# Kernel optimization log

Measured on AMD Instinct MI355X. Metric: run time of the kernel, lower is better.

Reference implementation:

```python
import jax, jax.numpy as jnp
import numpy as np
import math

B, D, N, H, NHEADS, NCLS = 4096, 256, 256, 1, 4, 10


def conv(x, w, b, stride, pad):
    y = jax.lax.conv_general_dilated(x, w, (stride, stride), [(pad, pad), (pad, pad)],
                                     dimension_numbers=('NCHW', 'OIHW', 'NCHW'))
    return y + b[None, :, None, None]


def cdist(z, c):
    # z: [B, D], c: [N, D] -> Euclidean distance [B, N]
    d2 = jnp.sum(z * z, -1)[:, None] + jnp.sum(c * c, -1)[None, :] - 2.0 * (z @ c.T)
    return jnp.sqrt(jnp.maximum(d2, 0.0))


def setup_inputs() -> dict:
    key = jax.random.key(0)
    ks = jax.random.split(key, 32)
    s = 0.02
    inp = {
        'x': jax.random.normal(ks[0], (B, 3, 32, 32), jnp.float32),
        'y': jax.random.randint(ks[1], (B,), 0, NCLS),
        'conv1_w': jax.random.normal(ks[2], (32, 3, 5, 5), jnp.float32) * s,
        'conv1_b': jnp.zeros((32,), jnp.float32),
        'conv2_w': jax.random.normal(ks[3], (64, 32, 3, 3), jnp.float32) * s,
        'conv2_b': jnp.zeros((64,), jnp.float32),
        'conv3_w': jax.random.normal(ks[4], (128, 64, 3, 3), jnp.float32) * s,
        'conv3_b': jnp.zeros((128,), jnp.float32),
        'conv4_w': jax.random.normal(ks[5], (256, 128, 3, 3), jnp.float32) * s,
        'conv4_b': jnp.zeros((256,), jnp.float32),
        'enc_w': jax.random.normal(ks[6], (256 * 8 * 8, D), jnp.float32) * s,
        'enc_b': jnp.zeros((D,), jnp.float32),
        'class_emb': jax.random.normal(ks[7], (NCLS, D), jnp.float32),
        'node_emb': jax.random.normal(ks[8], (N_NODES := 1, D), jnp.float32),
        'query_w': jax.random.normal(ks[9], (D, D), jnp.float32) * s,
        'query_b': jnp.zeros((D,), jnp.float32),
        'attn_w': jax.random.normal(ks[10], (D, D * NHEADS), jnp.float32) * s,
        'attn_b': jnp.zeros((D * NHEADS,), jnp.float32),
        'clf_w': jax.random.normal(ks[11], (D * NHEADS, NCLS), jnp.float32) * s,
        'clf_b': jnp.zeros((NCLS,), jnp.float32),
        'node_fc_w': jax.random.normal(ks[12], (D, D), jnp.float32) * s,
        'node_fc_b': jnp.zeros((D,), jnp.float32),
        'protos': jax.random.normal(ks[13], (N, D), jnp.float32),
        'grid_pos': jax.random.normal(ks[14], (N, D), jnp.float32),
        'temp_raw': jnp.array([math.log(0.95 / 0.05)], jnp.float32),
        'gate_logits': jnp.zeros((N,), jnp.float32),
    }
    return inp


def reference(x, y, conv1_w, conv1_b, conv2_w, conv2_b, conv3_w, conv3_b,
              conv4_w, conv4_b, enc_w, enc_b, class_emb, node_emb,
              query_w, query_b, attn_w, attn_b, clf_w, clf_b,
              node_fc_w, node_fc_b, protos, grid_pos, temp_raw, gate_logits):
    # shared encoder: conv stack -> flatten -> linear, 32x32 -> 8x8
    h1 = jax.nn.relu(conv(x, conv1_w, conv1_b, 2, 1))    # [B,32,15,15]
    h2 = jax.nn.relu(conv(h1, conv2_w, conv2_b, 2, 1))   # [B,64,8,8]
    h3 = jax.nn.relu(conv(h2, conv3_w, conv3_b, 1, 1))   # [B,128,8,8]
    h4 = jax.nn.relu(conv(h3, conv4_w, conv4_b, 1, 1))   # [B,256,8,8]
    z0 = h4.reshape(x.shape[0], -1) @ enc_w + enc_b      # [B,D]

    # Node: encoder_fc + SoftSOM (cdist + cdist -> softmax -> gate -> renorm -> blend)
    z = z0 @ node_fc_w + node_fc_b
    temp = jax.nn.sigmoid(temp_raw[0]) * (1.0 - 0.001) + 0.001
    d_total = cdist(z, protos) + cdist(z, grid_pos)      # [B,N]
    w = jax.nn.softmax(-d_total / temp, axis=-1) * jax.nn.sigmoid(gate_logits)[None, :]
    w = w / (w.sum(-1, keepdims=True) + 1e-8)
    blended = w @ protos                                 # [B,D]

    # node attention over n_nodes=1
    topo_stack = blended[:, None, :]                     # [B,1,D]
    query = class_emb[y] @ query_w + query_b             # [B,D]
    proj = (node_emb @ attn_w + attn_b).reshape(node_emb.shape[0], NHEADS, D)  # [n,h,D]
    attn_logits = jnp.einsum('bd,nhd->bhn', query, proj)
    attn_w_ = jax.nn.softmax(attn_logits, axis=-1)
    fused = jnp.einsum('bhn,bnd->bhd', attn_w_, topo_stack).reshape(x.shape[0], NHEADS * D)
    logits = fused @ clf_w + clf_b                       # [B,10]
    return logits
```

## Files before the change

kernel.cpp:

```cpp
#include <hip/hip_runtime.h>
#include <math.h>

#define TPB 256

typedef __attribute__((ext_vector_type(8))) short bf16x8;
typedef __attribute__((ext_vector_type(4))) float f32x4;
typedef __attribute__((ext_vector_type(2))) float f32x2;

#define OFF_PN2   0
#define OFF_GN2   256
#define OFF_GATE  512
#define OFF_TEMP  768
#define OFF_WEFF  1024
#define OFF_W1T   3584
#define OFF_W2T_BYTES 737280ul
#define OFF_W3T_BYTES 786432ul
#define OFF_W4T_BYTES 983040ul
#define OFF_EWT_BYTES 2097152ul
#define OFF_NFWT_BYTES 10485760ul
#define OFF_PJD_BYTES  10616832ul
#define OFF_GJD_BYTES  10747904ul
#define OFF_PTB_BYTES  10878976ul
#define OFF_A_BYTES   12582912ul
#define OFF_B_BYTES   (OFF_A_BYTES + 67108864ul)
#define OFF_Z0_BYTES  (OFF_B_BYTES + 33554432ul)

__device__ __forceinline__ float bf2f(ushort u) {
  return __uint_as_float(((unsigned)u) << 16);
}
__device__ __forceinline__ ushort f2bf(float f) {
  unsigned x = __float_as_uint(f);
  return (ushort)((x + 0x7fffu + ((x >> 16) & 1u)) >> 16);
}
__device__ __forceinline__ unsigned pack2(float a, float b) {
  return (unsigned)f2bf(a) | ((unsigned)f2bf(b) << 16);
}

__device__ __forceinline__ void gload_lds16(const ushort* g, ushort* l) {
  __builtin_amdgcn_global_load_lds(
      (const __attribute__((address_space(1))) unsigned int*)g,
      (__attribute__((address_space(3))) unsigned int*)l, 16, 0, 0);
}

__device__ __forceinline__ float block_sum(float v, float* red) {
  #pragma unroll
  for (int off = 32; off > 0; off >>= 1) v += __shfl_down(v, off, 64);
  int wid = threadIdx.x >> 6;
  __syncthreads();
  if ((threadIdx.x & 63) == 0) red[wid] = v;
  __syncthreads();
  return red[0] + red[1] + red[2] + red[3];
}

__global__ void __launch_bounds__(256) k_init(
    const float* __restrict__ ew,    ushort* __restrict__ ewt,
    const float* __restrict__ w1,    const float* __restrict__ w2,
    const float* __restrict__ w3,    const float* __restrict__ w4,
    float* __restrict__ w1t, ushort* __restrict__ w2t,
    ushort* __restrict__ w3t, ushort* __restrict__ w4t,
    const float* __restrict__ protos, const float* __restrict__ gridp,
    const float* __restrict__ gate_logits, const float* __restrict__ temp_raw,
    const float* __restrict__ clf_w, float* __restrict__ ws,
    float* __restrict__ z0,
    const float* __restrict__ nfw, ushort* __restrict__ nfwt,
    ushort* __restrict__ pjd, ushort* __restrict__ gjd,
    ushort* __restrict__ ptb) {
  __shared__ float tile[64][65];
  __shared__ float red[4];
  const int bx = blockIdx.x, t = threadIdx.x;

  if (bx < 1024) {
    int kb = bx & 255, nb = bx >> 8;
    #pragma unroll
    for (int i = 0; i < 16; ++i) {
      int idx = t + i*256, k = idx >> 6, n = idx & 63;
      tile[k][n] = ew[(size_t)(kb*64 + k)*256 + nb*64 + n];
    }
    __syncthreads();
    #pragma unroll
    for (int i = 0; i < 16; ++i) {
      int idx = t + i*256, n = idx >> 6, k = idx & 63;
      ewt[(size_t)(nb*64 + n)*16384 + kb*64 + k] = f2bf(tile[k][n]);
    }
    return;
  }
  if (bx < 2176) {
    int idx = (bx - 1024)*256 + t;
    if (idx < 2400) {
      int tap = idx >> 5, oc = idx & 31;
      w1t[idx] = w1[oc*75 + tap];
    }
    if (idx < 18432) {
      int tap = idx >> 11, r = idx & 2047, oc = r >> 5, ic = r & 31;
      w2t[idx] = f2bf(w2[oc*288 + ic*9 + tap]);
    }
    if (idx < 73728) {
      int tap = idx >> 13, r = idx & 8191, oc = r >> 6, ic = r & 63;
      w3t[idx] = f2bf(w3[oc*576 + ic*9 + tap]);
    }
    if (idx < 294912) {
      int tap = idx >> 15, r = idx & 32767, oc = r >> 7, ic = r & 127;
      w4t[idx] = f2bf(w4[oc*1152 + ic*9 + tap]);
    }
    return;
  }
  if (bx < 2432) {
    int b = bx - 2176;
    #pragma unroll
    for (int u = 0; u < 16; ++u) z0[(size_t)u*65536 + b*256 + t] = 0.f;
    float pv = protos[b*256 + t];
    float gv = gridp [b*256 + t];
    float sp = block_sum(pv*pv, red);
    float sg = block_sum(gv*gv, red);
    if (t == 0) {
      ws[OFF_PN2 + b] = sp;
      ws[OFF_GN2 + b] = sg;
      ws[OFF_GATE + b] = 1.f/(1.f + expf(-gate_logits[b]));
    }
    if (b == 0) {
      for (int i = t; i < 2560; i += TPB) {
        int d = i/10, c = i%10;
        ws[OFF_WEFF + i] = clf_w[d*10+c] + clf_w[(256+d)*10+c]
                         + clf_w[(512+d)*10+c] + clf_w[(768+d)*10+c];
      }
      if (t == 0) {
        float s = 1.f/(1.f + expf(-temp_raw[0]));
        ws[OFF_TEMP] = s*(1.f - 0.001f) + 0.001f;
      }
    }
    return;
  }
  {
    int idx = (bx - 2432)*256 + t;
    int a = idx >> 8, b = idx & 255;
    nfwt[idx] = f2bf(nfw[b*256 + a]);
    pjd [idx] = f2bf(protos[idx]);
    gjd [idx] = f2bf(gridp[idx]);
    ptb [idx] = f2bf(protos[b*256 + a]);
  }
}

__global__ void __launch_bounds__(256) k_conv12(const float* __restrict__ x,
    const float* __restrict__ w1t, const float* __restrict__ b1,
    const ushort* __restrict__ w2t, const float* __restrict__ b2,
    ushort* __restrict__ h2c) {
  __shared__ ushort xs[17*17*40];
  __shared__ float  xf[3*32*33];
  int b = blockIdx.x, t = threadIdx.x;
  for (int i = t; i < 5780; i += TPB) ((unsigned*)xs)[i] = 0u;
  const float* xb = x + (size_t)b*3072;
  #pragma unroll
  for (int i = 0; i < 3; ++i) {
    int idx = (t + i*256)*4;
    float4 v = *(const float4*)&xb[idx];
    int ic = idx >> 10, rem = idx & 1023, iy = rem >> 5, ix = rem & 31;
    float* dst = &xf[ic*1056 + iy*33 + ix];
    dst[0] = v.x; dst[1] = v.y; dst[2] = v.z; dst[3] = v.w;
  }
  __syncthreads();

  if (t < 225) {
    int oy = t/15, ox = t%15;
    f32x2 acc[16];
    #pragma unroll
    for (int o = 0; o < 16; ++o) acc[o] = *(const f32x2*)&b1[2*o];
    for (int ic = 0; ic < 3; ++ic) {
      const int icb = ic*1056;
      #pragma unroll
      for (int ky = 0; ky < 5; ++ky) {
        int iy = 2*oy - 1 + ky;
        bool rok = (unsigned)iy < 32u;
        int rbase = icb + (rok ? iy*33 : 0);
        #pragma unroll
        for (int kx = 0; kx < 5; ++kx) {
          int ix = 2*ox - 1 + kx;
          bool ok = rok && ((unsigned)ix < 32u);
          float xv = xf[rbase + (ok ? ix : 0)];
          xv = ok ? xv : 0.f;
          f32x2 xv2 = {xv, xv};
          const float* wrow = &w1t[(ic*25 + ky*5 + kx)*32];
          #pragma unroll
          for (int g = 0; g < 8; ++g) {
            f32x2 wlo = {wrow[4*g+0], wrow[4*g+1]};
            f32x2 whi = {wrow[4*g+2], wrow[4*g+3]};
            acc[2*g]   += xv2*wlo;
            acc[2*g+1] += xv2*whi;
          }
        }
      }
    }
    unsigned pk[16];
    #pragma unroll
    for (int g = 0; g < 16; ++g)
      pk[g] = pack2(fmaxf(acc[g].x, 0.f), fmaxf(acc[g].y, 0.f));
    ushort* cell = &xs[((oy+1)*17 + (ox+1))*40];
    #pragma unroll
    for (int q = 0; q < 4; ++q) *(uint4*)(cell + q*8) = ((uint4*)pk)[q];
  }
  __syncthreads();

  const int lane = t & 63, w = t >> 6;
  const int quad = lane >> 4, row16 = lane & 15;
  f32x4 acc2[4];
  #pragma unroll
  for (int mt = 0; mt < 4; ++mt) acc2[mt] = (f32x4)0.f;
  #pragma unroll
  for (int ky = 0; ky < 3; ++ky)
    #pragma unroll
    for (int kx = 0; kx < 3; ++kx) {
      int tap = ky*3 + kx;
      bf16x8 bf = *(const bf16x8*)&w2t[tap*2048 + (w*16 + row16)*32 + quad*8];
      #pragma unroll
      for (int mt = 0; mt < 4; ++mt) {
        int px = mt*16 + row16;
        int iy = 2*(px >> 3) + ky, ix = 2*(px & 7) + kx;
        bf16x8 af = *(const bf16x8*)&xs[(iy*17 + ix)*40 + quad*8];
        acc2[mt] = __builtin_amdgcn_mfma_f32_16x16x32_bf16(bf, af, acc2[mt], 0, 0, 0);
      }
    }
  float4 bb = *(const float4*)&b2[w*16 + quad*4];
  #pragma unroll
  for (int mt = 0; mt < 4; ++mt) {
    int px = mt*16 + row16;
    uint2 dd;
    dd.x = pack2(fmaxf(acc2[mt][0] + bb.x, 0.f), fmaxf(acc2[mt][1] + bb.y, 0.f));
    dd.y = pack2(fmaxf(acc2[mt][2] + bb.z, 0.f), fmaxf(acc2[mt][3] + bb.w, 0.f));
    *(uint2*)&h2c[(size_t)b*4096 + px*64 + w*16 + quad*4] = dd;
  }
}

__global__ void __launch_bounds__(256, 2) k_conv34(const ushort* __restrict__ h2c,
    const float* __restrict__ b3, const float* __restrict__ b4,
    const ushort* __restrict__ w3t, const ushort* __restrict__ w4t,
    ushort* __restrict__ h4c, int img_base) {
  __shared__ __attribute__((aligned(16))) ushort buf[27200];
  ushort* xp  = buf;
  ushort* h3p = buf;
  const int bl = blockIdx.x, t = threadIdx.x;

  for (int i = t; i < 648; i += 256) {
    int img = (i >= 324), r = i - img*324;
    int row = r/9, c = r - row*9;
    int rr = (row < 20) ? ((row < 10) ? row : row + 80)
                        : (((row-20) >> 1) + 1)*10 + ((row-20) & 1)*9;
    *(uint4*)&xp[img*7200 + rr*72 + c*8] = (uint4){0,0,0,0};
  }
  #pragma unroll
  for (int u = 0; u < 4; ++u) {
    int i = t + u*256;
    int img = i >> 9, px = (i >> 3) & 63, icg = i & 7;
    bf16x8 v = *(const bf16x8*)&h2c[(size_t)(img_base + bl*2 + img)*4096 + px*64 + icg*8];
    int row = ((px >> 3) + 1)*10 + (px & 7) + 1;
    *(bf16x8*)&xp[img*7200 + row*72 + icg*8] = v;
  }
  __syncthreads();

  const int lane = t & 63, w = t >> 6;
  const int quad = lane >> 4, row16 = lane & 15;

  int b3off[8], b4off[8], r11c[8];
  #pragma unroll
  for (int mt = 0; mt < 8; ++mt) {
    int px = (mt & 3)*16 + row16;
    int r00 = (px >> 3)*10 + (px & 7);
    int img = mt >> 2;
    b3off[mt] = img*7200  + r00*72  + quad*8;
    b4off[mt] = img*13600 + r00*136 + quad*8;
    r11c[mt]  = img*13600 + (r00 + 11)*136;
  }

  const int ocb3 = w*32;
  f32x4 c3[8][2];
  #pragma unroll
  for (int mt = 0; mt < 8; ++mt) { c3[mt][0] = (f32x4)0.f; c3[mt][1] = (f32x4)0.f; }
  const ushort* w3b = w3t + (ocb3 + row16)*64 + quad*8;
  bf16x8 wa0 = *(const bf16x8*)(w3b);
  bf16x8 wa1 = *(const bf16x8*)(w3b + 1024);
  #pragma unroll
  for (int tap = 0; tap < 9; ++tap) {
    const int t72 = ((tap/3)*10 + (tap%3))*72;
    #pragma unroll
    for (int ks = 0; ks < 2; ++ks) {
      const ushort* wn = w3b + ((ks == 0) ? (tap*8192 + 32) : ((tap+1)*8192));
      bf16x8 n0 = *(const bf16x8*)(wn);
      bf16x8 n1 = *(const bf16x8*)(wn + 1024);
      #pragma unroll
      for (int mt = 0; mt < 8; ++mt) {
        bf16x8 af = *(const bf16x8*)&xp[b3off[mt] + t72 + ks*32];
        c3[mt][0] = __builtin_amdgcn_mfma_f32_16x16x32_bf16(wa0, af, c3[mt][0], 0, 0, 0);
        c3[mt][1] = __builtin_amdgcn_mfma_f32_16x16x32_bf16(wa1, af, c3[mt][1], 0, 0, 0);
      }
      wa0 = n0; wa1 = n1;
    }
  }
  __syncthreads();

  for (int i = t; i < 1224; i += 256) {
    int img2 = (i >= 612), r = i - img2*612;
    int row = r/17, c = r - row*17;
    int rr = (row < 20) ? ((row < 10) ? row : row + 80)
                        : (((row-20) >> 1) + 1)*10 + ((row-20) & 1)*9;
    *(uint4*)&h3p[img2*13600 + rr*136 + c*8] = (uint4){0,0,0,0};
  }
  #pragma unroll
  for (int nt = 0; nt < 2; ++nt) {
    float4 bb = *(const float4*)&b3[ocb3 + nt*16 + quad*4];
    #pragma unroll
    for (int mt = 0; mt < 8; ++mt) {
      uint2 dd;
      dd.x = pack2(fmaxf(c3[mt][nt][0] + bb.x, 0.f), fmaxf(c3[mt][nt][1] + bb.y, 0.f));
      dd.y = pack2(fmaxf(c3[mt][nt][2] + bb.z, 0.f), fmaxf(c3[mt][nt][3] + bb.w, 0.f));
      *(uint2*)&h3p[r11c[mt] + ocb3 + nt*16 + quad*4] = dd;
    }
  }
  __syncthreads();

  const int ocb4 = w*64;
  f32x4 c4[8][4];
  #pragma unroll
  for (int mt = 0; mt < 8; ++mt)
    #pragma unroll
    for (int nt = 0; nt < 4; ++nt) c4[mt][nt] = (f32x4)0.f;
  const ushort* w4b = w4t + (ocb4 + row16)*128 + quad*8;
  bf16x8 r4[4];
  #pragma unroll
  for (int nt = 0; nt < 4; ++nt) r4[nt] = *(const bf16x8*)(w4b + nt*2048);
  #pragma unroll
  for (int tap = 0; tap < 9; ++tap) {
    const int t136 = ((tap/3)*10 + (tap%3))*136;
    #pragma unroll
    for (int ks = 0; ks < 4; ++ks) {
      const ushort* wn = w4b + ((ks < 3) ? (tap*32768 + (ks+1)*32) : ((tap+1)*32768));
      bf16x8 nx[4];
      #pragma unroll
      for (int nt = 0; nt < 4; ++nt) nx[nt] = *(const bf16x8*)(wn + nt*2048);
      #pragma unroll
      for (int mt = 0; mt < 8; ++mt) {
        bf16x8 ax = *(const bf16x8*)&h3p[b4off[mt] + t136 + ks*32];
        #pragma unroll
        for (int nt = 0; nt < 4; ++nt)
          c4[mt][nt] = __builtin_amdgcn_mfma_f32_16x16x32_bf16(ax, r4[nt], c4[mt][nt], 0, 0, 0);
      }
      #pragma unroll
      for (int nt = 0; nt < 4; ++nt) r4[nt] = nx[nt];
    }
  }
  #pragma unroll
  for (int nt = 0; nt < 4; ++nt) {
    int oc = ocb4 + nt*16 + row16;
    float bv = b4[oc];
    #pragma unroll
    for (int mt = 0; mt < 8; ++mt) {
      int ig = bl*2 + (mt >> 2);
      int px0 = (mt & 3)*16 + quad*4;
      uint2 dd;
      dd.x = pack2(fmaxf(c4[mt][nt][0] + bv, 0.f), fmaxf(c4[mt][nt][1] + bv, 0.f));
      dd.y = pack2(fmaxf(c4[mt][nt][2] + bv, 0.f), fmaxf(c4[mt][nt][3] + bv, 0.f));
      *(uint2*)&h4c[(size_t)ig*16384 + oc*64 + px0] = dd;
    }
  }
}

__global__ void __launch_bounds__(256) k_enc(const ushort* __restrict__ h4c,
    const ushort* __restrict__ ewt, float* __restrict__ z0, int img_base) {
  __shared__ ushort a_s[2][128*64];
  __shared__ ushort b_s[2][128*64];
  const int t = threadIdx.x, bid = blockIdx.x;
  const int grp = (bid & 7) + ((bid >> 7) << 3);
  const int slice = grp & 15;
  const int nb    = grp >> 4;
  const int mb    = (bid >> 3) & 15;
  const int M0 = mb*128, N0 = nb*128;
  const int kbase = slice*1024;
  const int lane = t & 63, wv = t >> 6;
  const int quad = lane >> 4, row16 = lane & 15;
  const int mrow0 = (wv & 1)*64, ncol0 = (wv >> 1)*64;
  const int sr = lane >> 3, sp = lane & 7;

  f32x4 acc[4][4];
  #pragma unroll
  for (int mt = 0; mt < 4; ++mt)
    #pragma unroll
    for (int nt = 0; nt < 4; ++nt) acc[mt][nt] = (f32x4)0.f;

  #pragma unroll
  for (int u = 0; u < 4; ++u) {
    int r = wv*32 + u*8 + sr;
    int c = sp ^ (r & 7);
    gload_lds16(&h4c[(size_t)(M0 + r)*16384 + kbase + c*8], &a_s[0][(wv*32 + u*8)*64]);
    gload_lds16(&ewt[(size_t)(N0 + r)*16384 + kbase + c*8], &b_s[0][(wv*32 + u*8)*64]);
  }
  __syncthreads();

  int cur = 0;
  for (int kt = 0; kt < 16; ++kt) {
    if (kt < 15) {
      const int k1 = kbase + (kt + 1)*64;
      #pragma unroll
      for (int u = 0; u < 4; ++u) {
        int r = wv*32 + u*8 + sr;
        int c = sp ^ (r & 7);
        gload_lds16(&h4c[(size_t)(M0 + r)*16384 + k1 + c*8], &a_s[cur^1][(wv*32 + u*8)*64]);
        gload_lds16(&ewt[(size_t)(N0 + r)*16384 + k1 + c*8], &b_s[cur^1][(wv*32 + u*8)*64]);
      }
    }
    #pragma unroll
    for (int ks = 0; ks < 2; ++ks) {
      bf16x8 af[4], bf[4];
      #pragma unroll
      for (int mt = 0; mt < 4; ++mt) {
        int r = mrow0 + mt*16 + row16;
        int p = (ks*4 + quad) ^ (r & 7);
        af[mt] = *(const bf16x8*)&a_s[cur][r*64 + p*8];
      }
      #pragma unroll
      for (int nt = 0; nt < 4; ++nt) {
        int r = ncol0 + nt*16 + row16;
        int p = (ks*4 + quad) ^ (r & 7);
        bf[nt] = *(const bf16x8*)&b_s[cur][r*64 + p*8];
      }
      #pragma unroll
      for (int mt = 0; mt < 4; ++mt)
        #pragma unroll
        for (int nt = 0; nt < 4; ++nt)
          acc[mt][nt] = __builtin_amdgcn_mfma_f32_16x16x32_bf16(af[mt], bf[nt], acc[mt][nt], 0, 0, 0);
    }
    __syncthreads();
    cur ^= 1;
  }
  #pragma unroll
  for (int mt = 0; mt < 4; ++mt) {
    int mrow = M0 + mrow0 + mt*16 + quad*4;
    #pragma unroll
    for (int nt = 0; nt < 4; ++nt) {
      int col = N0 + ncol0 + nt*16 + row16;
      #pragma unroll
      for (int r = 0; r < 4; ++r)
        atomicAdd(&z0[(size_t)(img_base + mrow + r)*256 + col], acc[mt][nt][r]);
    }
  }
}

__global__ void __launch_bounds__(256) k_post2(const float* __restrict__ z0,
    const float* __restrict__ enc_b, const float* __restrict__ nfb,
    const ushort* __restrict__ nfwt, const ushort* __restrict__ pjd,
    const ushort* __restrict__ gjd, const ushort* __restrict__ ptb,
    const float* __restrict__ ws, const float* __restrict__ clf_b,
    float* __restrict__ out) {
  __shared__ ushort zin[16*264];
  __shared__ ushort zS [16*264];
  __shared__ float  Df [16*264];
  __shared__ ushort wS [16*264];
  __shared__ float  weffS[2560];
  __shared__ float  gateS[256], pnS[256], gnS[256];
  __shared__ float  z2s[16];
  const int t = threadIdx.x, bx = blockIdx.x;
  const int img0 = bx*16;
  gateS[t] = ws[OFF_GATE + t];
  pnS[t]   = ws[OFF_PN2 + t];
  gnS[t]   = ws[OFF_GN2 + t];
  #pragma unroll
  for (int u = 0; u < 10; ++u)
    weffS[t + u*256] = ws[OFF_WEFF + t + u*256];
  #pragma unroll
  for (int u = 0; u < 16; ++u) {
    int i = t + u*256;
    int im = i >> 8, d = i & 255;
    zin[im*264 + d] = f2bf(z0[(size_t)(img0 + im)*256 + d] + enc_b[d]);
  }
  __syncthreads();

  const int lane = t & 63, w = t >> 6;
  const int quad = lane >> 4, row16 = lane & 15;
  const int n0 = w*64;

  f32x4 zC[4];
  #pragma unroll
  for (int nt = 0; nt < 4; ++nt) zC[nt] = (f32x4)0.f;
  #pragma unroll
  for (int ks = 0; ks < 8; ++ks) {
    bf16x8 az = *(const bf16x8*)&zin[row16*264 + ks*32 + quad*8];
    #pragma unroll
    for (int nt = 0; nt < 4; ++nt) {
      bf16x8 bw = *(const bf16x8*)&nfwt[(n0 + nt*16 + row16)*256 + ks*32 + quad*8];
      zC[nt] = __builtin_amdgcn_mfma_f32_16x16x32_bf16(az, bw, zC[nt], 0, 0, 0);
    }
  }
  #pragma unroll
  for (int nt = 0; nt < 4; ++nt) {
    int n = n0 + nt*16 + row16;
    float nb = nfb[n];
    #pragma unroll
    for (int r = 0; r < 4; ++r)
      zS[(quad*4 + r)*264 + n] = f2bf(zC[nt][r] + nb);
  }
  __syncthreads();

  {
    int im = t >> 4, jg = t & 15;
    float s = 0.f;
    #pragma unroll
    for (int q = 0; q < 16; ++q) {
      float v = bf2f(zS[im*264 + jg + 16*q]);
      s += v*v;
    }
    #pragma unroll
    for (int off = 8; off; off >>= 1) s += __shfl_xor(s, off, 16);
    if (jg == 0) z2s[im] = s;
  }
  __syncthreads();

  f32x4 dpC[4], dgC[4];
  #pragma unroll
  for (int nt = 0; nt < 4; ++nt) { dpC[nt] = (f32x4)0.f; dgC[nt] = (f32x4)0.f; }
  #pragma unroll
  for (int ks = 0; ks < 8; ++ks) {
    bf16x8 az = *(const bf16x8*)&zS[row16*264 + ks*32 + quad*8];
    #pragma unroll
    for (int nt = 0; nt < 4; ++nt) {
      int j = n0 + nt*16 + row16;
      bf16x8 bp = *(const bf16x8*)&pjd[j*256 + ks*32 + quad*8];
      bf16x8 bg = *(const bf16x8*)&gjd[j*256 + ks*32 + quad*8];
      dpC[nt] = __builtin_amdgcn_mfma_f32_16x16x32_bf16(az, bp, dpC[nt], 0, 0, 0);
      dgC[nt] = __builtin_amdgcn_mfma_f32_16x16x32_bf16(az, bg, dgC[nt], 0, 0, 0);
    }
  }
  {
    float temp = ws[OFF_TEMP];
    #pragma unroll
    for (int nt = 0; nt < 4; ++nt) {
      int j = n0 + nt*16 + row16;
      float pn = pnS[j], gn = gnS[j];
      #pragma unroll
      for (int r = 0; r < 4; ++r) {
        int im = quad*4 + r;
        float z2 = z2s[im];
        float d2p = z2 + pn - 2.f*dpC[nt][r];
        float d2g = z2 + gn - 2.f*dgC[nt][r];
        float l = -(sqrtf(fmaxf(d2p, 0.f)) + sqrtf(fmaxf(d2g, 0.f)))/temp;
        Df[im*264 + j] = l;
      }
    }
  }
  __syncthreads();

  {
    int im = t >> 4, jg = t & 15;
    float m = -1e30f;
    #pragma unroll
    for (int q = 0; q < 16; ++q) m = fmaxf(m, Df[im*264 + jg + 16*q]);
    #pragma unroll
    for (int off = 8; off; off >>= 1) m = fmaxf(m, __shfl_xor(m, off, 16));
    float E = 0.f, S = 0.f, ev[16], gv[16];
    #pragma unroll
    for (int q = 0; q < 16; ++q) {
      int j = jg + 16*q;
      float e = expf(Df[im*264 + j] - m);
      float g = gateS[j];
      ev[q] = e; gv[q] = g;
      E += e; S += e*g;
    }
    #pragma unroll
    for (int off = 8; off; off >>= 1) {
      E += __shfl_xor(E, off, 16);
      S += __shfl_xor(S, off, 16);
    }
    float inv = 1.f/(S + 1e-8f*E);
    #pragma unroll
    for (int q = 0; q < 16; ++q)
      wS[im*264 + jg + 16*q] = f2bf(ev[q]*gv[q]*inv);
  }
  __syncthreads();

  f32x4 blC[4];
  #pragma unroll
  for (int nt = 0; nt < 4; ++nt) blC[nt] = (f32x4)0.f;
  #pragma unroll
  for (int ks = 0; ks < 8; ++ks) {
    bf16x8 aw = *(const bf16x8*)&wS[row16*264 + ks*32 + quad*8];
    #pragma unroll
    for (int nt = 0; nt < 4; ++nt) {
      bf16x8 bp = *(const bf16x8*)&ptb[(n0 + nt*16 + row16)*256 + ks*32 + quad*8];
      blC[nt] = __builtin_amdgcn_mfma_f32_16x16x32_bf16(aw, bp, blC[nt], 0, 0, 0);
    }
  }
  #pragma unroll
  for (int nt = 0; nt < 4; ++nt) {
    int d = n0 + nt*16 + row16;
    #pragma unroll
    for (int r = 0; r < 4; ++r)
      Df[(quad*4 + r)*264 + d] = blC[nt][r];
  }
  __syncthreads();

  if (t < 160) {
    int im = t/10, c = t - im*10;
    float s = clf_b[c];
    for (int d = 0; d < 256; ++d)
      s += Df[im*264 + d]*weffS[d*10 + c];
    out[(size_t)(img0 + im)*10 + c] = s;
  }
}

extern "C" void kernel_launch(void* const* d_in, const int* in_sizes, int n_in,
                              void* d_out, int out_size, void* d_ws, size_t ws_size,
                              hipStream_t stream) {
  (void)in_sizes; (void)n_in; (void)out_size; (void)ws_size;
  const float* x      = (const float*)d_in[0];
  const float* c1w    = (const float*)d_in[2];
  const float* c1b    = (const float*)d_in[3];
  const float* c2w    = (const float*)d_in[4];
  const float* c2b    = (const float*)d_in[5];
  const float* c3w    = (const float*)d_in[6];
  const float* c3b    = (const float*)d_in[7];
  const float* c4w    = (const float*)d_in[8];
  const float* c4b    = (const float*)d_in[9];
  const float* encw   = (const float*)d_in[10];
  const float* encb   = (const float*)d_in[11];
  const float* clfw   = (const float*)d_in[18];
  const float* clfb   = (const float*)d_in[19];
  const float* nfw    = (const float*)d_in[20];
  const float* nfb    = (const float*)d_in[21];
  const float* protos = (const float*)d_in[22];
  const float* gridp  = (const float*)d_in[23];
  const float* traw   = (const float*)d_in[24];
  const float* gatel  = (const float*)d_in[25];

  float*  ws   = (float*)d_ws;
  float*  w1t  = ws + OFF_W1T;
  ushort* w2t  = (ushort*)((char*)d_ws + OFF_W2T_BYTES);
  ushort* w3t  = (ushort*)((char*)d_ws + OFF_W3T_BYTES);
  ushort* w4t  = (ushort*)((char*)d_ws + OFF_W4T_BYTES);
  ushort* ewt  = (ushort*)((char*)d_ws + OFF_EWT_BYTES);
  ushort* nfwt = (ushort*)((char*)d_ws + OFF_NFWT_BYTES);
  ushort* pjd  = (ushort*)((char*)d_ws + OFF_PJD_BYTES);
  ushort* gjd  = (ushort*)((char*)d_ws + OFF_GJD_BYTES);
  ushort* ptb  = (ushort*)((char*)d_ws + OFF_PTB_BYTES);
  ushort* h4c  = (ushort*)((char*)d_ws + OFF_A_BYTES);
  ushort* h2c  = (ushort*)((char*)d_ws + OFF_B_BYTES);
  float*  z0   = (float*) ((char*)d_ws + OFF_Z0_BYTES);
  float*  out  = (float*)d_out;

  hipLaunchKernelGGL(k_init, dim3(2688), dim3(TPB), 0, stream,
                     encw, ewt, c1w, c2w, c3w, c4w, w1t, w2t, w3t, w4t,
                     protos, gridp, gatel, traw, clfw, ws, z0,
                     nfw, nfwt, pjd, gjd, ptb);
  hipLaunchKernelGGL(k_conv12, dim3(4096), dim3(TPB), 0, stream, x, w1t, c1b, w2t, c2b, h2c);
  for (int c = 0; c < 2; ++c) {
    hipLaunchKernelGGL(k_conv34, dim3(1024), dim3(TPB), 0, stream,
                       h2c, c3b, c4b, w3t, w4t, h4c, c*2048);
    hipLaunchKernelGGL(k_enc, dim3(512), dim3(TPB), 0, stream, h4c, ewt, z0, c*2048);
  }
  hipLaunchKernelGGL(k_post2, dim3(256), dim3(TPB), 0, stream,
                     z0, encb, nfb, nfwt, pjd, gjd, ptb, ws, clfb, out);
}
```

Measured before the change: 518.9 us.

## Replace split-K atomic accumulation in encoder GEMM with partial buffers reduced in post

The encoder GEMM now uses 512-thread blocks, 8 K-slices of 2048 and 256 blocks per chunk. Each block writes its partial tile with plain stores into a per-slice buffer instead of doing fp32 atomicAdd into z0. k_post2 sums the 8 partials plus the bias when it loads z, so the z0 zero-init in k_init goes away. The aim is to remove atomic contention and the memset cost. In exchange, post-processing reads more memory, and the partial buffer reuses the already-consumed part of the h2c region.

```diff
diff --git a/kernel.cpp b/kernel.cpp
--- a/kernel.cpp
+++ b/kernel.cpp
@@ -61,7 +61,6 @@
     const float* __restrict__ protos, const float* __restrict__ gridp,
     const float* __restrict__ gate_logits, const float* __restrict__ temp_raw,
     const float* __restrict__ clf_w, float* __restrict__ ws,
-    float* __restrict__ z0,
     const float* __restrict__ nfw, ushort* __restrict__ nfwt,
     ushort* __restrict__ pjd, ushort* __restrict__ gjd,
     ushort* __restrict__ ptb) {
@@ -106,8 +105,6 @@
   }
   if (bx < 2432) {
     int b = bx - 2176;
-    #pragma unroll
-    for (int u = 0; u < 16; ++u) z0[(size_t)u*65536 + b*256 + t] = 0.f;
     float pv = protos[b*256 + t];
     float gv = gridp [b*256 + t];
     float sp = block_sum(pv*pv, red);
@@ -361,54 +358,53 @@
   }
 }
 
-__global__ void __launch_bounds__(256) k_enc(const ushort* __restrict__ h4c,
-    const ushort* __restrict__ ewt, float* __restrict__ z0, int img_base) {
+__global__ void __launch_bounds__(512) k_enc(const ushort* __restrict__ h4c,
+    const ushort* __restrict__ ewt, float* __restrict__ z0p) {
   __shared__ ushort a_s[2][128*64];
   __shared__ ushort b_s[2][128*64];
   const int t = threadIdx.x, bid = blockIdx.x;
-  const int grp = (bid & 7) + ((bid >> 7) << 3);
-  const int slice = grp & 15;
-  const int nb    = grp >> 4;
+  const int slice = bid & 7;
   const int mb    = (bid >> 3) & 15;
+  const int nb    = bid >> 7;
   const int M0 = mb*128, N0 = nb*128;
-  const int kbase = slice*1024;
+  const int kbase = slice*2048;
   const int lane = t & 63, wv = t >> 6;
   const int quad = lane >> 4, row16 = lane & 15;
-  const int mrow0 = (wv & 1)*64, ncol0 = (wv >> 1)*64;
+  const int mrow0 = (wv & 3)*32, ncol0 = (wv >> 2)*64;
   const int sr = lane >> 3, sp = lane & 7;
 
-  f32x4 acc[4][4];
-  #pragma unroll
-  for (int mt = 0; mt < 4; ++mt)
+  f32x4 acc[2][4];
+  #pragma unroll
+  for (int mt = 0; mt < 2; ++mt)
     #pragma unroll
     for (int nt = 0; nt < 4; ++nt) acc[mt][nt] = (f32x4)0.f;
 
   #pragma unroll
-  for (int u = 0; u < 4; ++u) {
-    int r = wv*32 + u*8 + sr;
+  for (int u = 0; u < 2; ++u) {
+    int r = wv*16 + u*8 + sr;
     int c = sp ^ (r & 7);
-    gload_lds16(&h4c[(size_t)(M0 + r)*16384 + kbase + c*8], &a_s[0][(wv*32 + u*8)*64]);
-    gload_lds16(&ewt[(size_t)(N0 + r)*16384 + kbase + c*8], &b_s[0][(wv*32 + u*8)*64]);
+    gload_lds16(&h4c[(size_t)(M0 + r)*16384 + kbase + c*8], &a_s[0][(wv*16 + u*8)*64]);
+    gload_lds16(&ewt[(size_t)(N0 + r)*16384 + kbase + c*8], &b_s[0][(wv*16 + u*8)*64]);
   }
   __syncthreads();
 
   int cur = 0;
-  for (int kt = 0; kt < 16; ++kt) {
-    if (kt < 15) {
+  for (int kt = 0; kt < 32; ++kt) {
+    if (kt < 31) {
       const int k1 = kbase + (kt + 1)*64;
       #pragma unroll
-      for (int u = 0; u < 4; ++u) {
-        int r = wv*32 + u*8 + sr;
+      for (int u = 0; u < 2; ++u) {
+        int r = wv*16 + u*8 + sr;
         int c = sp ^ (r & 7);
-        gload_lds16(&h4c[(size_t)(M0 + r)*16384 + k1 + c*8], &a_s[cur^1][(wv*32 + u*8)*64]);
-        gload_lds16(&ewt[(size_t)(N0 + r)*16384 + k1 + c*8], &b_s[cur^1][(wv*32 + u*8)*64]);
+        gload_lds16(&h4c[(size_t)(M0 + r)*16384 + k1 + c*8], &a_s[cur^1][(wv*16 + u*8)*64]);
+        gload_lds16(&ewt[(size_t)(N0 + r)*16384 + k1 + c*8], &b_s[cur^1][(wv*16 + u*8)*64]);
       }
     }
     #pragma unroll
     for (int ks = 0; ks < 2; ++ks) {
-      bf16x8 af[4], bf[4];
-      #pragma unroll
-      for (int mt = 0; mt < 4; ++mt) {
+      bf16x8 af[2], bf[4];
+      #pragma unroll
+      for (int mt = 0; mt < 2; ++mt) {
         int r = mrow0 + mt*16 + row16;
         int p = (ks*4 + quad) ^ (r & 7);
         af[mt] = *(const bf16x8*)&a_s[cur][r*64 + p*8];
@@ -420,7 +416,7 @@
         bf[nt] = *(const bf16x8*)&b_s[cur][r*64 + p*8];
       }
       #pragma unroll
-      for (int mt = 0; mt < 4; ++mt)
+      for (int mt = 0; mt < 2; ++mt)
         #pragma unroll
         for (int nt = 0; nt < 4; ++nt)
           acc[mt][nt] = __builtin_amdgcn_mfma_f32_16x16x32_bf16(af[mt], bf[nt], acc[mt][nt], 0, 0, 0);
@@ -429,19 +425,19 @@
     cur ^= 1;
   }
   #pragma unroll
-  for (int mt = 0; mt < 4; ++mt) {
-    int mrow = M0 + mrow0 + mt*16 + quad*4;
+  for (int mt = 0; mt < 2; ++mt) {
+    int il = M0 + mrow0 + mt*16 + quad*4;
     #pragma unroll
     for (int nt = 0; nt < 4; ++nt) {
       int col = N0 + ncol0 + nt*16 + row16;
       #pragma unroll
       for (int r = 0; r < 4; ++r)
-        atomicAdd(&z0[(size_t)(img_base + mrow + r)*256 + col], acc[mt][nt][r]);
-    }
-  }
-}
-
-__global__ void __launch_bounds__(256) k_post2(const float* __restrict__ z0,
+        z0p[((size_t)slice*2048 + il + r)*256 + col] = acc[mt][nt][r];
+    }
+  }
+}
+
+__global__ void __launch_bounds__(256) k_post2(const float* __restrict__ zp,
     const float* __restrict__ enc_b, const float* __restrict__ nfb,
     const ushort* __restrict__ nfwt, const ushort* __restrict__ pjd,
     const ushort* __restrict__ gjd, const ushort* __restrict__ ptb,
@@ -466,7 +462,13 @@
   for (int u = 0; u < 16; ++u) {
     int i = t + u*256;
     int im = i >> 8, d = i & 255;
-    zin[im*264 + d] = f2bf(z0[(size_t)(img0 + im)*256 + d] + enc_b[d]);
+    int img = img0 + im;
+    int cc = img >> 11, il = img & 2047;
+    const float* zb = zp + (size_t)cc*4194304 + (size_t)il*256 + d;
+    float s = enc_b[d];
+    #pragma unroll
+    for (int s8 = 0; s8 < 8; ++s8) s += zb[(size_t)s8*524288];
+    zin[im*264 + d] = f2bf(s);
   }
   __syncthreads();
 
@@ -638,19 +640,20 @@
   ushort* ptb  = (ushort*)((char*)d_ws + OFF_PTB_BYTES);
   ushort* h4c  = (ushort*)((char*)d_ws + OFF_A_BYTES);
   ushort* h2c  = (ushort*)((char*)d_ws + OFF_B_BYTES);
-  float*  z0   = (float*) ((char*)d_ws + OFF_Z0_BYTES);
+  float*  zp   = (float*) ((char*)d_ws + OFF_B_BYTES);
   float*  out  = (float*)d_out;
 
   hipLaunchKernelGGL(k_init, dim3(2688), dim3(TPB), 0, stream,
                      encw, ewt, c1w, c2w, c3w, c4w, w1t, w2t, w3t, w4t,
-                     protos, gridp, gatel, traw, clfw, ws, z0,
+                     protos, gridp, gatel, traw, clfw, ws,
                      nfw, nfwt, pjd, gjd, ptb);
   hipLaunchKernelGGL(k_conv12, dim3(4096), dim3(TPB), 0, stream, x, w1t, c1b, w2t, c2b, h2c);
   for (int c = 0; c < 2; ++c) {
     hipLaunchKernelGGL(k_conv34, dim3(1024), dim3(TPB), 0, stream,
                        h2c, c3b, c4b, w3t, w4t, h4c, c*2048);
-    hipLaunchKernelGGL(k_enc, dim3(512), dim3(TPB), 0, stream, h4c, ewt, z0, c*2048);
+    hipLaunchKernelGGL(k_enc, dim3(256), dim3(512), 0, stream,
+                       h4c, ewt, zp + (size_t)c*4194304);
   }
   hipLaunchKernelGGL(k_post2, dim3(256), dim3(TPB), 0, stream,
-                     z0, encb, nfb, nfwt, pjd, gjd, ptb, ws, clfb, out);
-}
+                     zp, encb, nfb, nfwt, pjd, gjd, ptb, ws, clfb, out);
+}
```

Result: faster. 495.2 us (-4.6%).
